# Kernel tuning notes

Measured on AMD Instinct MI355X. Metric: run time of the kernel, lower is better.

## Reference

```python
import jax, jax.numpy as jnp
import numpy as np

N = 100000
E = 1600000
F_IN = 3
H = 64


def setup_inputs() -> dict:
    key = jax.random.key(0)
    ks = jax.random.split(key, 12)
    x = jax.random.normal(ks[0], (N, F_IN), dtype=jnp.float32)
    edge_index = jax.random.randint(ks[1], (2, E), 0, N, dtype=jnp.int64)
    def glorot(k, fi, fo):
        s = jnp.sqrt(6.0 / (fi + fo)).astype(jnp.float32)
        return jax.random.uniform(k, (fi, fo), jnp.float32, -s, s)
    return {
        "x": x,
        "edge_index": edge_index,
        "W1": glorot(ks[2], F_IN, H), "b1": jnp.zeros((H,), jnp.float32),
        "W2": glorot(ks[3], H, H),   "b2": jnp.zeros((H,), jnp.float32),
        "W3": glorot(ks[4], H, H),   "b3": jnp.zeros((H,), jnp.float32),
        "Wh": glorot(ks[5], H, 1),   "bh": jnp.zeros((1,), jnp.float32),
    }


def _gcn_conv(x, src, dst, norm, W, b):
    # linear (no bias) -> gather by src -> scale by symmetric norm -> scatter-add to dst -> + bias
    h = x @ W                      # [N, F_out]
    msg = h[src] * norm[:, None]   # [E+N, F_out] (self-loops included)
    out = jax.ops.segment_sum(msg, dst, num_segments=N)
    return out + b


def reference(x, edge_index, W1, b1, W2, b2, W3, b3, Wh, bh):
    # add self-loops (PyG GCNConv default)
    loop = jnp.arange(N, dtype=edge_index.dtype)
    src = jnp.concatenate([edge_index[0], loop])
    dst = jnp.concatenate([edge_index[1], loop])
    # symmetric normalization deg^{-1/2}[src] * deg^{-1/2}[dst]
    deg = jax.ops.segment_sum(jnp.ones_like(dst, dtype=x.dtype), dst, num_segments=N)
    dinv = jnp.where(deg > 0, jax.lax.rsqrt(deg), 0.0)
    norm = dinv[src] * dinv[dst]

    h = _gcn_conv(x, src, dst, norm, W1, b1)
    h = jax.nn.relu(h)  # dropout is identity in eval mode
    h = _gcn_conv(h, src, dst, norm, W2, b2)
    h = jax.nn.relu(h)
    h = _gcn_conv(h, src, dst, norm, W3, b3)
    logits = (h @ Wh + bh).squeeze(-1)  # [N]
    return logits
```

## Files before the change

### kernel.cpp

```cpp
#include <hip/hip_runtime.h>


#define BKSH 8
#define EPB  4096

__device__ __forceinline__ float rlane(float v, int l) {
    return __int_as_float(__builtin_amdgcn_readlane(__float_as_int(v), l));
}
__device__ __forceinline__ int rfl(int v) { return __builtin_amdgcn_readfirstlane(v); }

__global__ void bhist(const int* __restrict__ dst, int* __restrict__ ghist,
                      int E, int NBK, int BLK) {
    __shared__ int h[512];
    int t = threadIdx.x, b = blockIdx.x;
    for (int i = t; i < NBK; i += 256) h[i] = 0;
    __syncthreads();
    int base = b * EPB;
    #pragma unroll
    for (int i = 0; i < 16; ++i) {
        int e = base + i * 256 + t;
        if (e < E) atomicAdd(&h[dst[e] >> BKSH], 1);
    }
    __syncthreads();
    for (int i = t; i < NBK; i += 256) ghist[(size_t)i * BLK + b] = h[i];
}

__global__ void gscan1(const int* __restrict__ in, int* __restrict__ out,
                       int* __restrict__ bsums, int M) {
    __shared__ int tmp[256];
    int i = blockIdx.x * 256 + threadIdx.x;
    int v = (i < M) ? in[i] : 0;
    tmp[threadIdx.x] = v; __syncthreads();
    for (int off = 1; off < 256; off <<= 1) {
        int t = (threadIdx.x >= off) ? tmp[threadIdx.x - off] : 0;
        __syncthreads();
        tmp[threadIdx.x] += t;
        __syncthreads();
    }
    if (i < M) out[i] = tmp[threadIdx.x] - v;
    if (threadIdx.x == 255) bsums[blockIdx.x] = tmp[255];
}

__global__ void gscan2(int* __restrict__ bsums, int nb) {
    __shared__ int tmp[1024];
    int v = (threadIdx.x < nb) ? bsums[threadIdx.x] : 0;
    tmp[threadIdx.x] = v; __syncthreads();
    for (int off = 1; off < 1024; off <<= 1) {
        int t = (threadIdx.x >= off) ? tmp[threadIdx.x - off] : 0;
        __syncthreads();
        tmp[threadIdx.x] += t;
        __syncthreads();
    }
    if (threadIdx.x < nb) bsums[threadIdx.x] = tmp[threadIdx.x] - v;
}

__global__ void bscatter(const int* __restrict__ src, const int* __restrict__ dst,
                         const int* __restrict__ goff, const int* __restrict__ gbsums,
                         uint2* __restrict__ tmp, int E, int NBK, int BLK) {
    __shared__ int off[512];
    int t = threadIdx.x, b = blockIdx.x;
    for (int i = t; i < NBK; i += 256) {
        size_t m = (size_t)i * BLK + b;
        off[i] = goff[m] + gbsums[m >> 8];
    }
    __syncthreads();
    int base = b * EPB;
    #pragma unroll
    for (int i = 0; i < 16; ++i) {
        int e = base + i * 256 + t;
        if (e < E) {
            int d = dst[e];
            int p = atomicAdd(&off[d >> BKSH], 1);
            tmp[p] = make_uint2((unsigned)src[e], (unsigned)d);
        }
    }
}

__global__ void bucketA(const uint2* __restrict__ tmp, const int* __restrict__ goff,
                        const int* __restrict__ gbsums, int* __restrict__ rowptr,
                        float* __restrict__ dinv, int N, int NBK, int BLK, int E) {
    __shared__ int lc[256], sc[256];
    int b = blockIdx.x, t = threadIdx.x;
    lc[t] = 0; __syncthreads();
    size_t m0 = (size_t)b * BLK;
    int p0 = goff[m0] + gbsums[m0 >> 8];
    int p1 = E;
    if (b + 1 < NBK) { size_t m1 = (size_t)(b + 1) * BLK; p1 = goff[m1] + gbsums[m1 >> 8]; }
    for (int p = p0 + t; p < p1; p += 256) atomicAdd(&lc[tmp[p].y & 255], 1);
    __syncthreads();
    int v = lc[t];
    sc[t] = v; __syncthreads();
    for (int off = 1; off < 256; off <<= 1) {
        int tv = (t >= off) ? sc[t - off] : 0;
        __syncthreads();
        sc[t] += tv;
        __syncthreads();
    }
    int node = (b << BKSH) + t;
    if (node < N) {
        rowptr[node] = p0 + (sc[t] - v);
        dinv[node]   = rsqrtf((float)(v + 1));
    }
    if (b == 0 && t == 0) rowptr[N] = E;
}

__global__ void fillB(const uint2* __restrict__ tmp, const int* __restrict__ goff,
                      const int* __restrict__ gbsums, const int* __restrict__ rowptr,
                      const float* __restrict__ dinv, const float* __restrict__ x,
                      float2* __restrict__ ew, float4* __restrict__ a1,
                      int N, int NBK, int BLK, int E) {
    __shared__ int   lfill[256];
    __shared__ int   rbase[257];
    __shared__ float ldv[256];
    int b = blockIdx.x, t = threadIdx.x;
    int node0 = b << BKSH;
    lfill[t] = 0;
    int node = node0 + t;
    rbase[t] = rowptr[min(node, N)];
    ldv[t]   = dinv[min(node, N - 1)];
    if (t == 0) rbase[256] = rowptr[min(node0 + 256, N)];
    __syncthreads();
    size_t m0 = (size_t)b * BLK;
    int p0 = goff[m0] + gbsums[m0 >> 8];
    int p1 = E;
    if (b + 1 < NBK) { size_t m1 = (size_t)(b + 1) * BLK; p1 = goff[m1] + gbsums[m1 >> 8]; }
    for (int p = p0 + t; p < p1; p += 256) {
        uint2 e = tmp[p];
        int s = (int)e.x, dl = (int)(e.y & 255);
        float w = dinv[s] * ldv[dl];
        int pos = rbase[dl] + atomicAdd(&lfill[dl], 1);
        ew[pos] = make_float2(__int_as_float(s), w);
    }
    __syncthreads();
    int grp = t >> 4, sub = t & 15;
    for (int ni = grp; ni < 256; ni += 16) {
        int n = node0 + ni;
        if (n >= N) break;
        int q0 = rbase[ni], q1 = rbase[ni + 1];
        float ax = 0.f, ay = 0.f, az = 0.f;
        for (int p = q0 + sub; p < q1; p += 16) {
            float2 e = ew[p];
            int s = __float_as_int(e.x);
            ax = fmaf(e.y, x[s*3+0], ax);
            ay = fmaf(e.y, x[s*3+1], ay);
            az = fmaf(e.y, x[s*3+2], az);
        }
        #pragma unroll
        for (int off = 8; off; off >>= 1) {
            ax += __shfl_down(ax, off, 16);
            ay += __shfl_down(ay, off, 16);
            az += __shfl_down(az, off, 16);
        }
        if (sub == 0) {
            float dv = ldv[ni], sw = dv * dv;
            a1[n] = make_float4(fmaf(sw, x[n*3+0], ax),
                                fmaf(sw, x[n*3+1], ay),
                                fmaf(sw, x[n*3+2], az), sw);
        }
    }
}

__global__ void fold_head(const float* __restrict__ W3, const float* __restrict__ b3,
                          const float* __restrict__ Wh, const float* __restrict__ bh,
                          float* __restrict__ wc) {
    int k = threadIdx.x;
    float acc = 0.0f;
    for (int f = 0; f < 64; f++) acc += W3[k*64+f] * Wh[f];
    wc[k] = acc;
    if (k == 0) {
        float bb = bh[0];
        for (int f = 0; f < 64; f++) bb += b3[f] * Wh[f];
        wc[64] = bb;
    }
}

__global__ void fused_l2l3(const float2* __restrict__ ew, const int* __restrict__ rowptr,
                           const float4* __restrict__ a1, const float* __restrict__ W1,
                           const float* __restrict__ b1, const float* __restrict__ W2,
                           const float* __restrict__ b2, const float* __restrict__ wc,
                           float* __restrict__ z, int N, int E) {
    __shared__ float  Wl[64*64];
    __shared__ float4 pay[4][64];
    __shared__ float  a2buf[4][64];
    const int tid = threadIdx.x;
    for (int i = tid; i < 4096; i += 256) Wl[i] = W2[i];
    const int lane = tid & 63;
    const int wv   = tid >> 6;
    const float w10 = W1[lane], w11 = W1[64+lane], w12 = W1[128+lane];
    const float b1f = b1[lane], b2f = b2[lane], wcf = wc[lane];
    const int NPW = 8;
    const int n0 = (blockIdx.x * 4 + wv) * NPW;
    int   rpl = rowptr[min(n0 + lane, N)];
    float4 sg = a1[min(n0 + lane, N - 1)];
    __syncthreads();
    if (n0 >= N) return;
    for (int cur = 0; cur < NPW; ++cur) {
        int n = n0 + cur;
        if (n >= N) break;
        int p0 = rfl(__shfl(rpl, cur));
        int p1 = rfl(__shfl(rpl, cur + 1));
        float sx = rlane(sg.x, cur), sy = rlane(sg.y, cur);
        float sz2 = rlane(sg.z, cur), sw = rlane(sg.w, cur);
        float ts = fmaf(sz2, w12, fmaf(sy, w11, fmaf(sx, w10, b1f)));
        float acc = sw * fmaxf(ts, 0.f);
        for (int pc = p0; pc < p1; pc += 64) {
            int pidx = pc + lane; if (pidx >= p1) pidx = p1 - 1;
            float2 e = ew[pidx];
            float4 g = a1[__float_as_int(e.x)];
            pay[wv][lane] = make_float4(g.x, g.y, g.z, e.y);
            int m = p1 - pc; if (m > 64) m = 64;
            const float4* pp = (const float4*)&pay[wv][0];
            int j = 0;
            for (; j + 3 < m; j += 4) {
                float4 P0 = pp[j], P1 = pp[j+1], P2 = pp[j+2], P3 = pp[j+3];
                float t0 = fmaf(P0.z, w12, fmaf(P0.y, w11, fmaf(P0.x, w10, b1f)));
                float t1 = fmaf(P1.z, w12, fmaf(P1.y, w11, fmaf(P1.x, w10, b1f)));
                float t2 = fmaf(P2.z, w12, fmaf(P2.y, w11, fmaf(P2.x, w10, b1f)));
                float t3 = fmaf(P3.z, w12, fmaf(P3.y, w11, fmaf(P3.x, w10, b1f)));
                acc = fmaf(P0.w, fmaxf(t0, 0.f), acc);
                acc = fmaf(P1.w, fmaxf(t1, 0.f), acc);
                acc = fmaf(P2.w, fmaxf(t2, 0.f), acc);
                acc = fmaf(P3.w, fmaxf(t3, 0.f), acc);
            }
            for (; j < m; ++j) {
                float4 P = pp[j];
                float tt = fmaf(P.z, w12, fmaf(P.y, w11, fmaf(P.x, w10, b1f)));
                acc = fmaf(P.w, fmaxf(tt, 0.f), acc);
            }
        }
        a2buf[wv][lane] = acc;
        float h = b2f;
        const float4* a4 = (const float4*)&a2buf[wv][0];
        #pragma unroll
        for (int k4 = 0; k4 < 16; ++k4) {
            float4 a = a4[k4];
            h = fmaf(a.x, Wl[(4*k4+0)*64 + lane], h);
            h = fmaf(a.y, Wl[(4*k4+1)*64 + lane], h);
            h = fmaf(a.z, Wl[(4*k4+2)*64 + lane], h);
            h = fmaf(a.w, Wl[(4*k4+3)*64 + lane], h);
        }
        float v = fmaxf(h, 0.f) * wcf;
        #pragma unroll
        for (int off = 32; off; off >>= 1) v += __shfl_down(v, off);
        if (lane == 0) z[n] = v;
    }
}

__global__ void final_wave(const float* __restrict__ z, const float2* __restrict__ ew,
                           const int* __restrict__ rowptr, const float* __restrict__ dinv,
                           const float* __restrict__ wc, float* __restrict__ out, int N) {
    int g   = (blockIdx.x * blockDim.x + threadIdx.x) >> 4;
    int sub = threadIdx.x & 15;
    if (g >= N) return;
    int p0 = rowptr[g], p1 = rowptr[g+1];
    float acc = 0.f;
    for (int p = p0 + sub; p < p1; p += 16) {
        float2 e = ew[p];
        acc = fmaf(e.y, z[__float_as_int(e.x)], acc);
    }
    #pragma unroll
    for (int off = 8; off; off >>= 1) acc += __shfl_down(acc, off, 16);
    if (sub == 0) {
        float dv = dinv[g];
        out[g] = fmaf(dv * dv, z[g], acc) + wc[64];
    }
}

extern "C" void kernel_launch(void* const* d_in, const int* in_sizes, int n_in,
                              void* d_out, int out_size, void* d_ws, size_t ws_size,
                              hipStream_t stream) {
    const float* x   = (const float*)d_in[0];
    const int*   ei  = (const int*)d_in[1];
    const float* W1  = (const float*)d_in[2];
    const float* b1  = (const float*)d_in[3];
    const float* W2  = (const float*)d_in[4];
    const float* b2  = (const float*)d_in[5];
    const float* W3  = (const float*)d_in[6];
    const float* b3  = (const float*)d_in[7];
    const float* Wh  = (const float*)d_in[8];
    const float* bh  = (const float*)d_in[9];
    float* logits = (float*)d_out;

    const int N = in_sizes[0] / 3;
    const int E = in_sizes[1] / 2;
    const int* src = ei;
    const int* dst = ei + E;

    const int NBK = (N + 255) >> BKSH;
    const int BLK = (E + EPB - 1) / EPB;
    const int M   = NBK * BLK;

    float* base = (float*)d_ws;
    size_t o = 0;
    float*  dinv   = base + o; o += (size_t)N;
    o = (o + 3) & ~(size_t)3;
    float4* a1     = (float4*)(base + o); o += (size_t)4*N;
    int*    rowptr = (int*)(base + o); o += (size_t)N + 1;
    int*    gbsums = (int*)(base + o); o += 1024;
    o = (o + 1) & ~(size_t)1;
    float2* ew     = (float2*)(base + o); o += (size_t)2*E;
    uint2*  tmpb   = (uint2*)(base + o); o += (size_t)2*E;
    float*  zbuf   = base + o; o += (size_t)N;
    float*  wc     = base + o; o += 65;
    int*    ghist  = (int*)(base + o); o += (size_t)M;
    int*    goff   = (int*)(base + o); o += (size_t)M;

    const int BS = 256;
    int gM   = (M + BS - 1) / BS;
    int g16  = ((size_t)N * 16 + BS - 1) / BS;
    int gFU  = (N + 31) / 32;

    bhist    <<<BLK, BS, 0, stream>>>(dst, ghist, E, NBK, BLK);
    gscan1   <<<gM,  BS, 0, stream>>>(ghist, goff, gbsums, M);
    gscan2   <<<1, 1024, 0, stream>>>(gbsums, gM);
    bscatter <<<BLK, BS, 0, stream>>>(src, dst, goff, gbsums, tmpb, E, NBK, BLK);
    bucketA  <<<NBK, BS, 0, stream>>>(tmpb, goff, gbsums, rowptr, dinv, N, NBK, BLK, E);
    fillB    <<<NBK, BS, 0, stream>>>(tmpb, goff, gbsums, rowptr, dinv, x, ew, a1, N, NBK, BLK, E);

    fold_head  <<<1, 64, 0, stream>>>(W3, b3, Wh, bh, wc);
    fused_l2l3 <<<gFU, BS, 0, stream>>>(ew, rowptr, a1, W1, b1, W2, b2, wc, zbuf, N, E);
    final_wave <<<g16, BS, 0, stream>>>(zbuf, ew, rowptr, dinv, wc, logits, N);
}
```

Before: 164.6 us.

## Batch edge gathers across a wave's nodes and prefetch the next chunk

The per-node gather loop in the fused layer kernel is replaced by a loop that walks the combined edge range of all 8 nodes a wave owns, in 64-edge windows. Each window fills all lanes even when nodes have few edges, and the next window's edge and feature loads are issued before the current window is reduced, overlapping gather latency with compute. The cost is more complex control flow, extra live registers, and a trailing loop for nodes left without edges.

```diff
diff --git a/kernel.cpp b/kernel.cpp
--- a/kernel.cpp
+++ b/kernel.cpp
@@ -7,7 +7,9 @@
 __device__ __forceinline__ float rlane(float v, int l) {
     return __int_as_float(__builtin_amdgcn_readlane(__float_as_int(v), l));
 }
-__device__ __forceinline__ int rfl(int v) { return __builtin_amdgcn_readfirstlane(v); }
+__device__ __forceinline__ int rlane_i(int v, int l) {
+    return __builtin_amdgcn_readlane(v, l);
+}
 
 __global__ void bhist(const int* __restrict__ dst, int* __restrict__ ghist,
                       int E, int NBK, int BLK) {
@@ -194,40 +196,80 @@
     float4 sg = a1[min(n0 + lane, N - 1)];
     __syncthreads();
     if (n0 >= N) return;
-    for (int cur = 0; cur < NPW; ++cur) {
-        int n = n0 + cur;
-        if (n >= N) break;
-        int p0 = rfl(__shfl(rpl, cur));
-        int p1 = rfl(__shfl(rpl, cur + 1));
-        float sx = rlane(sg.x, cur), sy = rlane(sg.y, cur);
-        float sz2 = rlane(sg.z, cur), sw = rlane(sg.w, cur);
-        float ts = fmaf(sz2, w12, fmaf(sy, w11, fmaf(sx, w10, b1f)));
-        float acc = sw * fmaxf(ts, 0.f);
-        for (int pc = p0; pc < p1; pc += 64) {
-            int pidx = pc + lane; if (pidx >= p1) pidx = p1 - 1;
-            float2 e = ew[pidx];
-            float4 g = a1[__float_as_int(e.x)];
-            pay[wv][lane] = make_float4(g.x, g.y, g.z, e.y);
-            int m = p1 - pc; if (m > 64) m = 64;
-            const float4* pp = (const float4*)&pay[wv][0];
-            int j = 0;
-            for (; j + 3 < m; j += 4) {
-                float4 P0 = pp[j], P1 = pp[j+1], P2 = pp[j+2], P3 = pp[j+3];
-                float t0 = fmaf(P0.z, w12, fmaf(P0.y, w11, fmaf(P0.x, w10, b1f)));
-                float t1 = fmaf(P1.z, w12, fmaf(P1.y, w11, fmaf(P1.x, w10, b1f)));
-                float t2 = fmaf(P2.z, w12, fmaf(P2.y, w11, fmaf(P2.x, w10, b1f)));
-                float t3 = fmaf(P3.z, w12, fmaf(P3.y, w11, fmaf(P3.x, w10, b1f)));
-                acc = fmaf(P0.w, fmaxf(t0, 0.f), acc);
-                acc = fmaf(P1.w, fmaxf(t1, 0.f), acc);
-                acc = fmaf(P2.w, fmaxf(t2, 0.f), acc);
-                acc = fmaf(P3.w, fmaxf(t3, 0.f), acc);
+    int NPWv = N - n0; if (NPWv > NPW) NPWv = NPW;
+    const int P0 = rlane_i(rpl, 0);
+    const int P8 = rlane_i(rpl, NPW);
+    int cur = 0;
+    float sx = rlane(sg.x, 0), sy = rlane(sg.y, 0);
+    float sz2 = rlane(sg.z, 0), sw = rlane(sg.w, 0);
+    float ts = fmaf(sz2, w12, fmaf(sy, w11, fmaf(sx, w10, b1f)));
+    float acc = sw * fmaxf(ts, 0.f);
+    int pos = P0;
+    float2 e_c = make_float2(0.f, 0.f); float4 g_c = make_float4(0.f,0.f,0.f,0.f);
+    if (P0 < P8) {
+        int pidx = P0 + lane; if (pidx >= P8) pidx = P8 - 1;
+        e_c = ew[pidx];
+        g_c = a1[__float_as_int(e_c.x)];
+    }
+    for (int wbase = P0; wbase < P8; wbase += 64) {
+        pay[wv][lane] = make_float4(g_c.x, g_c.y, g_c.z, e_c.y);
+        int wend = wbase + 64; if (wend > P8) wend = P8;
+        int nb = wbase + 64;
+        if (nb < P8) {
+            int pidx = nb + lane; if (pidx >= P8) pidx = P8 - 1;
+            e_c = ew[pidx];
+            g_c = a1[__float_as_int(e_c.x)];
+        }
+        const float4* pp = (const float4*)&pay[wv][0];
+        bool more = true;
+        while (more && cur < NPWv) {
+            int p1 = rlane_i(rpl, cur + 1);
+            int segend = p1 < wend ? p1 : wend;
+            int j = pos - wbase, jend = segend - wbase;
+            for (; j + 3 < jend; j += 4) {
+                float4 Q0 = pp[j], Q1 = pp[j+1], Q2 = pp[j+2], Q3 = pp[j+3];
+                float t0 = fmaf(Q0.z, w12, fmaf(Q0.y, w11, fmaf(Q0.x, w10, b1f)));
+                float t1 = fmaf(Q1.z, w12, fmaf(Q1.y, w11, fmaf(Q1.x, w10, b1f)));
+                float t2 = fmaf(Q2.z, w12, fmaf(Q2.y, w11, fmaf(Q2.x, w10, b1f)));
+                float t3 = fmaf(Q3.z, w12, fmaf(Q3.y, w11, fmaf(Q3.x, w10, b1f)));
+                acc = fmaf(Q0.w, fmaxf(t0, 0.f), acc);
+                acc = fmaf(Q1.w, fmaxf(t1, 0.f), acc);
+                acc = fmaf(Q2.w, fmaxf(t2, 0.f), acc);
+                acc = fmaf(Q3.w, fmaxf(t3, 0.f), acc);
             }
-            for (; j < m; ++j) {
-                float4 P = pp[j];
-                float tt = fmaf(P.z, w12, fmaf(P.y, w11, fmaf(P.x, w10, b1f)));
-                acc = fmaf(P.w, fmaxf(tt, 0.f), acc);
+            for (; j < jend; ++j) {
+                float4 Q = pp[j];
+                float tt = fmaf(Q.z, w12, fmaf(Q.y, w11, fmaf(Q.x, w10, b1f)));
+                acc = fmaf(Q.w, fmaxf(tt, 0.f), acc);
             }
-        }
+            pos = segend;
+            if (p1 <= wend) {
+                a2buf[wv][lane] = acc;
+                float h = b2f;
+                const float4* a4 = (const float4*)&a2buf[wv][0];
+                #pragma unroll
+                for (int k4 = 0; k4 < 16; ++k4) {
+                    float4 a = a4[k4];
+                    h = fmaf(a.x, Wl[(4*k4+0)*64 + lane], h);
+                    h = fmaf(a.y, Wl[(4*k4+1)*64 + lane], h);
+                    h = fmaf(a.z, Wl[(4*k4+2)*64 + lane], h);
+                    h = fmaf(a.w, Wl[(4*k4+3)*64 + lane], h);
+                }
+                float v = fmaxf(h, 0.f) * wcf;
+                #pragma unroll
+                for (int off = 32; off; off >>= 1) v += __shfl_down(v, off);
+                if (lane == 0) z[n0 + cur] = v;
+                cur++;
+                if (cur < NPWv) {
+                    sx = rlane(sg.x, cur); sy = rlane(sg.y, cur);
+                    sz2 = rlane(sg.z, cur); sw = rlane(sg.w, cur);
+                    ts = fmaf(sz2, w12, fmaf(sy, w11, fmaf(sx, w10, b1f)));
+                    acc = sw * fmaxf(ts, 0.f);
+                } else more = false;
+            } else more = false;
+        }
+    }
+    while (cur < NPWv) {
         a2buf[wv][lane] = acc;
         float h = b2f;
         const float4* a4 = (const float4*)&a2buf[wv][0];
@@ -242,7 +284,14 @@
         float v = fmaxf(h, 0.f) * wcf;
         #pragma unroll
         for (int off = 32; off; off >>= 1) v += __shfl_down(v, off);
-        if (lane == 0) z[n] = v;
+        if (lane == 0) z[n0 + cur] = v;
+        cur++;
+        if (cur < NPWv) {
+            sx = rlane(sg.x, cur); sy = rlane(sg.y, cur);
+            sz2 = rlane(sg.z, cur); sw = rlane(sg.w, cur);
+            ts = fmaf(sz2, w12, fmaf(sy, w11, fmaf(sx, w10, b1f)));
+            acc = sw * fmaxf(ts, 0.f);
+        }
     }
 }
 
```

Measured after the change: 166.0 us. About the same (+0.9%).

## Factor symmetric norm into per-node scaling and store source indices only

Applied to the files above, without the earlier changes.

The per-edge weight dinv[src]*dinv[dst] is replaced by pre-scaling node features with dinv on the source side and applying dinv[dst] once after aggregation. The edge array then holds only source ints instead of (src, weight) pairs, which halves edge-list traffic in the layer-1, layer-2/3 and final gathers. A pre-scaled float4 copy of x is added, and the fused kernel moves to 1024-thread blocks with 16 waves sharing one W2 load. Reassociating the normalization changes floating-point rounding slightly.

```diff
diff --git a/kernel.cpp b/kernel.cpp
--- a/kernel.cpp
+++ b/kernel.cpp
@@ -7,7 +7,9 @@
 __device__ __forceinline__ float rlane(float v, int l) {
     return __int_as_float(__builtin_amdgcn_readlane(__float_as_int(v), l));
 }
-__device__ __forceinline__ int rfl(int v) { return __builtin_amdgcn_readfirstlane(v); }
+__device__ __forceinline__ int rlane_i(int v, int l) {
+    return __builtin_amdgcn_readlane(v, l);
+}
 
 __global__ void bhist(const int* __restrict__ dst, int* __restrict__ ghist,
                       int E, int NBK, int BLK) {
@@ -77,8 +79,9 @@
 }
 
 __global__ void bucketA(const uint2* __restrict__ tmp, const int* __restrict__ goff,
-                        const int* __restrict__ gbsums, int* __restrict__ rowptr,
-                        float* __restrict__ dinv, int N, int NBK, int BLK, int E) {
+                        const int* __restrict__ gbsums, const float* __restrict__ x,
+                        int* __restrict__ rowptr, float* __restrict__ dinv,
+                        float4* __restrict__ xd4, int N, int NBK, int BLK, int E) {
     __shared__ int lc[256], sc[256];
     int b = blockIdx.x, t = threadIdx.x;
     lc[t] = 0; __syncthreads();
@@ -99,15 +102,18 @@
     int node = (b << BKSH) + t;
     if (node < N) {
         rowptr[node] = p0 + (sc[t] - v);
-        dinv[node]   = rsqrtf((float)(v + 1));
+        float dvv = rsqrtf((float)(v + 1));
+        dinv[node] = dvv;
+        xd4[node]  = make_float4(dvv * x[3*node], dvv * x[3*node+1],
+                                 dvv * x[3*node+2], 0.f);
     }
     if (b == 0 && t == 0) rowptr[N] = E;
 }
 
 __global__ void fillB(const uint2* __restrict__ tmp, const int* __restrict__ goff,
                       const int* __restrict__ gbsums, const int* __restrict__ rowptr,
-                      const float* __restrict__ dinv, const float* __restrict__ x,
-                      float2* __restrict__ ew, float4* __restrict__ a1,
+                      const float* __restrict__ dinv, const float4* __restrict__ xd4,
+                      int* __restrict__ ewsrc, float4* __restrict__ a1,
                       int N, int NBK, int BLK, int E) {
     __shared__ int   lfill[256];
     __shared__ int   rbase[257];
@@ -127,9 +133,8 @@
     for (int p = p0 + t; p < p1; p += 256) {
         uint2 e = tmp[p];
         int s = (int)e.x, dl = (int)(e.y & 255);
-        float w = dinv[s] * ldv[dl];
         int pos = rbase[dl] + atomicAdd(&lfill[dl], 1);
-        ew[pos] = make_float2(__int_as_float(s), w);
+        ewsrc[pos] = s;
     }
     __syncthreads();
     int grp = t >> 4, sub = t & 15;
@@ -139,11 +144,8 @@
         int q0 = rbase[ni], q1 = rbase[ni + 1];
         float ax = 0.f, ay = 0.f, az = 0.f;
         for (int p = q0 + sub; p < q1; p += 16) {
-            float2 e = ew[p];
-            int s = __float_as_int(e.x);
-            ax = fmaf(e.y, x[s*3+0], ax);
-            ay = fmaf(e.y, x[s*3+1], ay);
-            az = fmaf(e.y, x[s*3+2], az);
+            float4 xs = xd4[ewsrc[p]];
+            ax += xs.x; ay += xs.y; az += xs.z;
         }
         #pragma unroll
         for (int off = 8; off; off >>= 1) {
@@ -152,10 +154,10 @@
             az += __shfl_down(az, off, 16);
         }
         if (sub == 0) {
-            float dv = ldv[ni], sw = dv * dv;
-            a1[n] = make_float4(fmaf(sw, x[n*3+0], ax),
-                                fmaf(sw, x[n*3+1], ay),
-                                fmaf(sw, x[n*3+2], az), sw);
+            float dv = ldv[ni];
+            float4 xn = xd4[n];
+            a1[n] = make_float4(dv * (ax + xn.x), dv * (ay + xn.y),
+                                dv * (az + xn.z), dv);
         }
     }
 }
@@ -174,22 +176,22 @@
     }
 }
 
-__global__ void fused_l2l3(const float2* __restrict__ ew, const int* __restrict__ rowptr,
+__global__ void fused_l2l3(const int* __restrict__ ewsrc, const int* __restrict__ rowptr,
                            const float4* __restrict__ a1, const float* __restrict__ W1,
                            const float* __restrict__ b1, const float* __restrict__ W2,
                            const float* __restrict__ b2, const float* __restrict__ wc,
-                           float* __restrict__ z, int N, int E) {
+                           float* __restrict__ zz, int N, int E) {
     __shared__ float  Wl[64*64];
-    __shared__ float4 pay[4][64];
-    __shared__ float  a2buf[4][64];
+    __shared__ float4 pay[16][64];
+    __shared__ float  a2buf[16][64];
     const int tid = threadIdx.x;
-    for (int i = tid; i < 4096; i += 256) Wl[i] = W2[i];
+    for (int i = tid; i < 4096; i += 1024) Wl[i] = W2[i];
     const int lane = tid & 63;
     const int wv   = tid >> 6;
     const float w10 = W1[lane], w11 = W1[64+lane], w12 = W1[128+lane];
     const float b1f = b1[lane], b2f = b2[lane], wcf = wc[lane];
     const int NPW = 8;
-    const int n0 = (blockIdx.x * 4 + wv) * NPW;
+    const int n0 = (blockIdx.x * 16 + wv) * NPW;
     int   rpl = rowptr[min(n0 + lane, N)];
     float4 sg = a1[min(n0 + lane, N - 1)];
     __syncthreads();
@@ -197,17 +199,17 @@
     for (int cur = 0; cur < NPW; ++cur) {
         int n = n0 + cur;
         if (n >= N) break;
-        int p0 = rfl(__shfl(rpl, cur));
-        int p1 = rfl(__shfl(rpl, cur + 1));
+        int p0 = rlane_i(rpl, cur);
+        int p1 = rlane_i(rpl, cur + 1);
         float sx = rlane(sg.x, cur), sy = rlane(sg.y, cur);
         float sz2 = rlane(sg.z, cur), sw = rlane(sg.w, cur);
         float ts = fmaf(sz2, w12, fmaf(sy, w11, fmaf(sx, w10, b1f)));
         float acc = sw * fmaxf(ts, 0.f);
         for (int pc = p0; pc < p1; pc += 64) {
             int pidx = pc + lane; if (pidx >= p1) pidx = p1 - 1;
-            float2 e = ew[pidx];
-            float4 g = a1[__float_as_int(e.x)];
-            pay[wv][lane] = make_float4(g.x, g.y, g.z, e.y);
+            int s = ewsrc[pidx];
+            float4 g = a1[s];
+            pay[wv][lane] = g;
             int m = p1 - pc; if (m > 64) m = 64;
             const float4* pp = (const float4*)&pay[wv][0];
             int j = 0;
@@ -228,6 +230,7 @@
                 acc = fmaf(P.w, fmaxf(tt, 0.f), acc);
             }
         }
+        acc *= sw;
         a2buf[wv][lane] = acc;
         float h = b2f;
         const float4* a4 = (const float4*)&a2buf[wv][0];
@@ -242,11 +245,11 @@
         float v = fmaxf(h, 0.f) * wcf;
         #pragma unroll
         for (int off = 32; off; off >>= 1) v += __shfl_down(v, off);
-        if (lane == 0) z[n] = v;
-    }
-}
-
-__global__ void final_wave(const float* __restrict__ z, const float2* __restrict__ ew,
+        if (lane == 0) zz[n] = sw * v;
+    }
+}
+
+__global__ void final_wave(const float* __restrict__ zz, const int* __restrict__ ewsrc,
                            const int* __restrict__ rowptr, const float* __restrict__ dinv,
                            const float* __restrict__ wc, float* __restrict__ out, int N) {
     int g   = (blockIdx.x * blockDim.x + threadIdx.x) >> 4;
@@ -255,14 +258,12 @@
     int p0 = rowptr[g], p1 = rowptr[g+1];
     float acc = 0.f;
     for (int p = p0 + sub; p < p1; p += 16) {
-        float2 e = ew[p];
-        acc = fmaf(e.y, z[__float_as_int(e.x)], acc);
+        acc += zz[ewsrc[p]];
     }
     #pragma unroll
     for (int off = 8; off; off >>= 1) acc += __shfl_down(acc, off, 16);
     if (sub == 0) {
-        float dv = dinv[g];
-        out[g] = fmaf(dv * dv, z[g], acc) + wc[64];
+        out[g] = fmaf(dinv[g], zz[g] + acc, wc[64]);
     }
 }
 
@@ -295,12 +296,14 @@
     float*  dinv   = base + o; o += (size_t)N;
     o = (o + 3) & ~(size_t)3;
     float4* a1     = (float4*)(base + o); o += (size_t)4*N;
+    float4* xd4    = (float4*)(base + o); o += (size_t)4*N;
     int*    rowptr = (int*)(base + o); o += (size_t)N + 1;
     int*    gbsums = (int*)(base + o); o += 1024;
     o = (o + 1) & ~(size_t)1;
-    float2* ew     = (float2*)(base + o); o += (size_t)2*E;
+    int*    ewsrc  = (int*)(base + o); o += (size_t)E;
+    o = (o + 1) & ~(size_t)1;
     uint2*  tmpb   = (uint2*)(base + o); o += (size_t)2*E;
-    float*  zbuf   = base + o; o += (size_t)N;
+    float*  zz     = base + o; o += (size_t)N;
     float*  wc     = base + o; o += 65;
     int*    ghist  = (int*)(base + o); o += (size_t)M;
     int*    goff   = (int*)(base + o); o += (size_t)M;
@@ -308,16 +311,16 @@
     const int BS = 256;
     int gM   = (M + BS - 1) / BS;
     int g16  = ((size_t)N * 16 + BS - 1) / BS;
-    int gFU  = (N + 31) / 32;
+    int gFU  = (N + 127) / 128;
 
     bhist    <<<BLK, BS, 0, stream>>>(dst, ghist, E, NBK, BLK);
     gscan1   <<<gM,  BS, 0, stream>>>(ghist, goff, gbsums, M);
     gscan2   <<<1, 1024, 0, stream>>>(gbsums, gM);
     bscatter <<<BLK, BS, 0, stream>>>(src, dst, goff, gbsums, tmpb, E, NBK, BLK);
-    bucketA  <<<NBK, BS, 0, stream>>>(tmpb, goff, gbsums, rowptr, dinv, N, NBK, BLK, E);
-    fillB    <<<NBK, BS, 0, stream>>>(tmpb, goff, gbsums, rowptr, dinv, x, ew, a1, N, NBK, BLK, E);
+    bucketA  <<<NBK, BS, 0, stream>>>(tmpb, goff, gbsums, x, rowptr, dinv, xd4, N, NBK, BLK, E);
+    fillB    <<<NBK, BS, 0, stream>>>(tmpb, goff, gbsums, rowptr, dinv, xd4, ewsrc, a1, N, NBK, BLK, E);
 
     fold_head  <<<1, 64, 0, stream>>>(W3, b3, Wh, bh, wc);
-    fused_l2l3 <<<gFU, BS, 0, stream>>>(ew, rowptr, a1, W1, b1, W2, b2, wc, zbuf, N, E);
-    final_wave <<<g16, BS, 0, stream>>>(zbuf, ew, rowptr, dinv, wc, logits, N);
-}
+    fused_l2l3 <<<gFU, 1024, 0, stream>>>(ewsrc, rowptr, a1, W1, b1, W2, b2, wc, zz, N, E);
+    final_wave <<<g16, BS, 0, stream>>>(zz, ewsrc, rowptr, dinv, wc, logits, N);
+}
```

Result: no change. 166.4 us (+1.1%).
